# Kernel tuning notes

Measured on AMD Instinct MI355X. Metric: run time of the kernel, lower is better.

Reference implementation:

```python
import jax, jax.numpy as jnp
import numpy as np

B, N, E, H, F, L, S = 4, 384, 768, 32, 3072, 12, 512
D = E // H


def setup_inputs() -> dict:
    key = jax.random.key(0)
    ks = jax.random.split(key, 32)
    inp = {}
    # forward args
    inp['node_type'] = jax.random.randint(ks[0], (B, N, 1), 1, S + 1)  # table has S+1 rows; 0 = pad (unused)
    inp['node_input_feature'] = jax.random.normal(ks[1], (B, N, E), jnp.float32)
    inp['in_degree'] = jax.random.randint(ks[2], (B, N), 0, S)
    inp['out_degree'] = jax.random.randint(ks[3], (B, N), 0, S)
    inp['attn_bias'] = jax.random.normal(ks[4], (B, N, N), jnp.float32) * 0.1
    inp['spatial_pos'] = jax.random.randint(ks[5], (B, N, N), 0, S)
    # embedding tables (normal stddev 0.02, as in the flax module)
    inp['node_emb'] = jax.random.normal(ks[6], (S + 1, E), jnp.float32) * 0.02
    inp['in_deg_emb'] = jax.random.normal(ks[7], (S, E), jnp.float32) * 0.02
    inp['out_deg_emb'] = jax.random.normal(ks[8], (S, E), jnp.float32) * 0.02
    inp['sp_emb'] = jax.random.normal(ks[9], (S, H), jnp.float32) * 0.02
    inp['sp_emb_rev'] = jax.random.normal(ks[10], (S, H), jnp.float32) * 0.02
    # per-layer weights, stacked along leading L axis
    se, sf = 1.0 / np.sqrt(E), 1.0 / np.sqrt(F)
    inp['Wq'] = jax.random.normal(ks[11], (L, E, E), jnp.float32) * se
    inp['bq'] = jax.random.normal(ks[12], (L, E), jnp.float32) * se
    inp['Wk'] = jax.random.normal(ks[13], (L, E, E), jnp.float32) * se
    inp['bk'] = jax.random.normal(ks[14], (L, E), jnp.float32) * se
    inp['Wv'] = jax.random.normal(ks[15], (L, E, E), jnp.float32) * se
    inp['bv'] = jax.random.normal(ks[16], (L, E), jnp.float32) * se
    inp['Wo'] = jax.random.normal(ks[17], (L, E, E), jnp.float32) * se
    inp['bo'] = jnp.zeros((L, E), jnp.float32)
    inp['W1'] = jax.random.normal(ks[18], (L, E, F), jnp.float32) * se
    inp['b1'] = jax.random.normal(ks[19], (L, F), jnp.float32) * se
    inp['W2'] = jax.random.normal(ks[20], (L, F, E), jnp.float32) * sf
    inp['b2'] = jax.random.normal(ks[21], (L, E), jnp.float32) * sf
    inp['ln1_s'] = jnp.ones((L, E), jnp.float32)
    inp['ln1_b'] = jnp.zeros((L, E), jnp.float32)
    inp['ln2_s'] = jnp.ones((L, E), jnp.float32)
    inp['ln2_b'] = jnp.zeros((L, E), jnp.float32)
    return inp


def _layernorm(x, scale, bias, eps=1e-5):
    m = x.mean(-1, keepdims=True)
    v = ((x - m) ** 2).mean(-1, keepdims=True)
    return (x - m) / jnp.sqrt(v + eps) * scale + bias


def _encoder(node_type, node_input_feature, in_degree, out_degree, attn_bias, spatial_pos,
             node_emb, in_deg_emb, out_deg_emb, sp_emb, sp_emb_rev,
             Wq, bq, Wk, bk, Wv, bv, Wo, bo, W1, b1, W2, b2, ln1_s, ln1_b, ln2_s, ln2_b):
    nt = node_type[..., 0]                               # [B,N]
    padding_mask = nt == 0                               # [B,N]
    # node features: node_emb(node_type).sum(-2) + degree embeddings + input feature
    x = (node_emb[node_type].sum(axis=-2)
         + in_deg_emb[in_degree] + out_deg_emb[out_degree]
         + node_input_feature)                           # [B,N,E]
    # spatial attention bias: [B,N,N,H] -> [B,H,N,N], plus graph-level attn_bias
    sb = sp_emb[spatial_pos] + sp_emb_rev[jnp.transpose(spatial_pos, (0, 2, 1))]
    bias = jnp.transpose(sb, (0, 3, 1, 2)) + attn_bias[:, None]  # [B,H,N,N]

    x = jnp.transpose(x, (1, 0, 2))                      # [N,B,E]
    scaling = D ** (-0.5)
    neg_inf = jnp.float32(-jnp.inf)

    def layer(x, p):
        wq, bq_, wk, bk_, wv, bv_, wo, bo_, w1, b1_, w2, b2_, s1, t1, s2, t2 = p
        q = ((x @ wq) + bq_) * scaling                   # [N,B,E], bias scaled too (faithful)
        k = (x @ wk) + bk_
        v = (x @ wv) + bv_
        q = q.reshape(N, B, H, D)
        k = k.reshape(N, B, H, D)
        v = v.reshape(N, B, H, D)
        w = jnp.einsum('nbhd,mbhd->bhnm', q, k) + bias   # [B,H,N,N]
        w = jnp.where(padding_mask[:, None, None, :], neg_inf, w)
        probs = jax.nn.softmax(w.astype(jnp.float32), axis=-1).astype(x.dtype)
        a = jnp.einsum('bhnm,mbhd->nbhd', probs, v).reshape(N, B, E)
        a = a @ wo + bo_
        x = _layernorm(x + a, s1, t1)                    # post-LN
        h = jax.nn.gelu(x @ w1 + b1_)                    # approximate gelu (flax default)
        h = h @ w2 + b2_
        x = _layernorm(x + h, s2, t2)
        return x, None

    xs = (Wq, bq, Wk, bk, Wv, bv, Wo, bo, W1, b1, W2, b2, ln1_s, ln1_b, ln2_s, ln2_b)
    x, _ = jax.lax.scan(layer, x, xs)
    return x                                             # [N,B,E]


def reference(node_type, node_input_feature, in_degree, out_degree, attn_bias, spatial_pos,
              node_emb, in_deg_emb, out_deg_emb, sp_emb, sp_emb_rev,
              Wq, bq, Wk, bk, Wv, bv, Wo, bo, W1, b1, W2, b2, ln1_s, ln1_b, ln2_s, ln2_b):
    return _encoder(node_type, node_input_feature, in_degree, out_degree, attn_bias, spatial_pos,
                    node_emb, in_deg_emb, out_deg_emb, sp_emb, sp_emb_rev,
                    Wq, bq, Wk, bk, Wv, bv, Wo, bo, W1, b1, W2, b2, ln1_s, ln1_b, ln2_s, ln2_b)
```

## Files before the change

### kernel.cpp

```cpp
#include <hip/hip_runtime.h>
#include <hip/hip_bf16.h>

#define Bb 4
#define Nn 384
#define Ee 768
#define Hh 32
#define Ff 3072
#define Ll 12
#define Ss 512
#define Mm (Nn*Bb)

typedef __attribute__((ext_vector_type(8))) short bf16x8;
typedef __attribute__((ext_vector_type(4))) float f32x4;
typedef unsigned short u16;

__device__ __forceinline__ u16 f2b(float f) {
  union { float f; unsigned int i; } c; c.f = f;
  unsigned int x = c.i;
  return (u16)((x + 0x7fffu + ((x >> 16) & 1u)) >> 16);
}
__device__ __forceinline__ float b2f(u16 u) {
  union { unsigned int i; float f; } c; c.i = ((unsigned int)u) << 16; return c.f;
}
__device__ __forceinline__ unsigned pkcvt(float lo, float hi) {
  unsigned r;
  asm("v_cvt_pk_bf16_f32 %0, %1, %2" : "=v"(r) : "v"(lo), "v"(hi));
  return r;
}
__device__ __forceinline__ void gload_lds16(const void* g, void* l) {
  __builtin_amdgcn_global_load_lds((__attribute__((address_space(1))) void*)(g),
                                   (__attribute__((address_space(3))) void*)(l), 16, 0, 0);
}

__global__ __launch_bounds__(256) void embed_kernel(
    const int* __restrict__ node_type, const float* __restrict__ nif,
    const int* __restrict__ in_deg, const int* __restrict__ out_deg,
    const float* __restrict__ node_emb, const float* __restrict__ ind_emb,
    const float* __restrict__ outd_emb,
    float* __restrict__ x, u16* __restrict__ xb)
{
  const int r = blockIdx.x;
  const int n = r / Bb, b = r % Bb;
  const int nt  = node_type[b*Nn + n];
  const int idg = in_deg[b*Nn + n];
  const int odg = out_deg[b*Nn + n];
  for (int c = threadIdx.x; c < Ee; c += 256) {
    float val = node_emb[(size_t)nt*Ee + c] + ind_emb[(size_t)idg*Ee + c]
              + outd_emb[(size_t)odg*Ee + c] + nif[((size_t)b*Nn + n)*Ee + c];
    x[(size_t)r*Ee + c] = val;
    xb[(size_t)r*Ee + c] = f2b(val);
  }
}

__global__ void spT_kernel(const int* __restrict__ sp, int* __restrict__ spT)
{
  __shared__ int tile[32][33];
  const int b = blockIdx.z;
  const int n0 = blockIdx.y * 32, m0 = blockIdx.x * 32;
  const int tx = threadIdx.x, ty = threadIdx.y;
  for (int i = ty; i < 32; i += 8)
    tile[i][tx] = sp[((size_t)b*Nn + n0 + i)*Nn + m0 + tx];
  __syncthreads();
  for (int i = ty; i < 32; i += 8)
    spT[((size_t)b*Nn + m0 + i)*Nn + n0 + tx] = tile[tx][i];
}

__global__ __launch_bounds__(256) void bias_pre_kernel(
    const float* __restrict__ atb, const int* __restrict__ sp, const int* __restrict__ spT,
    const float* __restrict__ sp_emb, const float* __restrict__ sp_emb_rev,
    u16* __restrict__ biasb)
{
  __shared__ float spc[512], sprc[512];
  const int bx = blockIdx.x, h = blockIdx.y, b = blockIdx.z;
  const int t = threadIdx.x;
  for (int i = t; i < 512; i += 256) {
    spc[i]  = sp_emb[(size_t)i*Hh + h];
    sprc[i] = sp_emb_rev[(size_t)i*Hh + h];
  }
  __syncthreads();
  const int q = bx*16 + ((t >> 2) & 15);
  const size_t rowb = ((size_t)b*Nn + q)*Nn;
  u16* outb = biasb + (((size_t)(b*Hh + h)*24 + bx)*24)*256 + t;
  const int mbase = ((t >> 6) << 2) + (t & 3);
  for (int tt = 0; tt < 24; ++tt) {
    const int m = tt*16 + mbase;
    float v = atb[rowb + m] + spc[sp[rowb + m]] + sprc[spT[rowb + m]];
    outb[tt*256] = f2b(v);
  }
}

__global__ __launch_bounds__(256) void wconv_kernel(
    const float* __restrict__ Wq, const float* __restrict__ Wk, const float* __restrict__ Wv,
    const float* __restrict__ Wo, const float* __restrict__ W1, const float* __restrict__ W2,
    int layer0, u16* __restrict__ wTall, unsigned slotStride)
{
  __shared__ float tile[64][68];
  const int layer = layer0 + blockIdx.y;
  u16* slot = wTall + (size_t)blockIdx.y * slotStride;
  int tid = blockIdx.x;
  const float* src; u16* dst; int Ns, Ks;
  if (tid < 432)       { int seg = tid / 144; tid -= seg*144;
                         src = (seg==0?Wq:(seg==1?Wk:Wv)) + (size_t)layer*Ee*Ee;
                         dst = slot + (size_t)seg*589824; Ns = 768; Ks = 768; }
  else if (tid < 576)  { tid -= 432; src = Wo + (size_t)layer*Ee*Ee; dst = slot + 1769472; Ns = 768;  Ks = 768; }
  else if (tid < 1152) { tid -= 576; src = W1 + (size_t)layer*Ee*Ff; dst = slot + 2359296; Ns = 3072; Ks = 768; }
  else                 { tid -= 1152; src = W2 + (size_t)layer*Ff*Ee; dst = slot + 4718592; Ns = 768; Ks = 3072; }
  const int tc = Ns >> 6;
  const int tk = tid / tc, tn = tid % tc;
  const int t = threadIdx.x;
  #pragma unroll
  for (int i = 0; i < 4; ++i) {
    const int id = t + i*256;
    const int r = id >> 4, c = (id & 15) << 2;
    *(float4*)&tile[r][c] = *(const float4*)(src + (size_t)(tk*64 + r)*Ns + tn*64 + c);
  }
  __syncthreads();
  #pragma unroll
  for (int i = 0; i < 2; ++i) {
    const int ch = t + i*256;
    const int n = ch >> 3, kc = (ch & 7) << 3;
    uint4 u;
    u.x = pkcvt(tile[kc+0][n], tile[kc+1][n]);
    u.y = pkcvt(tile[kc+2][n], tile[kc+3][n]);
    u.z = pkcvt(tile[kc+4][n], tile[kc+5][n]);
    u.w = pkcvt(tile[kc+6][n], tile[kc+7][n]);
    *(uint4*)(dst + (size_t)(tn*64 + n)*Ks + tk*64 + kc) = u;
  }
}

template<int EPI>
__global__ __launch_bounds__(256) void gemm3_kernel(
    const u16* __restrict__ A, const u16* __restrict__ Bw,
    const float* __restrict__ b0, const float* __restrict__ b1, const float* __restrict__ b2,
    int Kfull, int Kc, float scaleQ,
    float* __restrict__ outF, u16* __restrict__ outB)
{
  __shared__ __align__(16) u16 As[2][64][64];
  __shared__ __align__(16) u16 Bs[2][64][64];
  const int t = threadIdx.x, lane = t & 63, wave = t >> 6;
  int bx = blockIdx.x, by = blockIdx.y;
  {
    const int gx = gridDim.x;
    const int nwg = gx * gridDim.y;
    const int bid = bx + gx * by;
    const int cpx = nwg >> 3;
    const int s = (bid & 7) * cpx + (bid >> 3);
    bx = s % gx; by = s / gx;
  }
  const int m0 = bx * 64, n0 = by * 64;
  const int k0 = blockIdx.z * Kc;
  const int wm = wave >> 1, wn = wave & 1;
  const int ql = lane & 15, hi = lane >> 4;
  const int nk = Kc >> 6;
  const int sr = t >> 3;
  const int sslot = (t & 7) ^ (sr & 7);
  const size_t aoff = (size_t)(m0 + sr)*Kfull + k0 + (sslot << 3);
  const size_t boff = (size_t)(n0 + sr)*Kfull + k0 + (sslot << 3);
  const size_t rstep = (size_t)32 * Kfull;

  f32x4 acc[2][2];
  #pragma unroll
  for (int a = 0; a < 2; ++a)
    #pragma unroll
    for (int c = 0; c < 2; ++c) acc[a][c] = (f32x4){0.f,0.f,0.f,0.f};

  gload_lds16(A + aoff,         (char*)&As[0][0][0] + t*16);
  gload_lds16(A + aoff + rstep, (char*)&As[0][0][0] + 4096 + t*16);
  gload_lds16(Bw + boff,         (char*)&Bs[0][0][0] + t*16);
  gload_lds16(Bw + boff + rstep, (char*)&Bs[0][0][0] + 4096 + t*16);

  for (int kt = 0; kt < nk; ++kt) {
    const int cur = kt & 1, nxt = cur ^ 1;
    const bool pre = (kt + 1 < nk);
    if (pre) {
      const size_t kk = (size_t)(kt + 1) << 6;
      gload_lds16(A + aoff + kk,         (char*)&As[nxt][0][0] + t*16);
      gload_lds16(A + aoff + kk + rstep, (char*)&As[nxt][0][0] + 4096 + t*16);
      gload_lds16(Bw + boff + kk,         (char*)&Bs[nxt][0][0] + t*16);
      gload_lds16(Bw + boff + kk + rstep, (char*)&Bs[nxt][0][0] + 4096 + t*16);
      asm volatile("s_waitcnt vmcnt(4)" ::: "memory");
    } else {
      asm volatile("s_waitcnt vmcnt(0)" ::: "memory");
    }
    __builtin_amdgcn_s_barrier();
    __builtin_amdgcn_sched_barrier(0);

    const char* aBase = (const char*)&As[cur][0][0];
    const char* bBase = (const char*)&Bs[cur][0][0];
    bf16x8 af[2][2], bf[2][2];
    #pragma unroll
    for (int f = 0; f < 2; ++f)
      #pragma unroll
      for (int ks = 0; ks < 2; ++ks) {
        const int row = wm*32 + f*16 + ql;
        af[f][ks] = *(const bf16x8*)(aBase + row*128 + ((((ks<<2)+hi) ^ (ql&7)) << 4));
      }
    #pragma unroll
    for (int f = 0; f < 2; ++f)
      #pragma unroll
      for (int ks = 0; ks < 2; ++ks) {
        const int row = wn*32 + f*16 + ql;
        bf[f][ks] = *(const bf16x8*)(bBase + row*128 + ((((ks<<2)+hi) ^ (ql&7)) << 4));
      }
    #pragma unroll
    for (int ks = 0; ks < 2; ++ks)
      #pragma unroll
      for (int fm = 0; fm < 2; ++fm)
        #pragma unroll
        for (int fn = 0; fn < 2; ++fn)
          acc[fm][fn] = __builtin_amdgcn_mfma_f32_16x16x32_bf16(af[fm][ks], bf[fn][ks], acc[fm][fn], 0, 0, 0);
    if (pre) {
      __builtin_amdgcn_sched_barrier(0);
      __builtin_amdgcn_s_barrier();
    }
  }

  #pragma unroll
  for (int fm = 0; fm < 2; ++fm) {
    const int rowb = m0 + wm*32 + fm*16 + hi*4;
    #pragma unroll
    for (int fn = 0; fn < 2; ++fn) {
      const int gcol = n0 + wn*32 + fn*16 + ql;
      float bv, scale = 1.0f;
      if (EPI == 0) {
        const int seg = gcol / 768;
        const int cw = gcol - seg*768;
        bv = (seg == 0) ? b0[cw] : ((seg == 1) ? b1[cw] : b2[cw]);
        if (seg == 0) scale = scaleQ;
      } else if (EPI == 1) {
        bv = (blockIdx.z == 0) ? b0[gcol] : 0.0f;
      } else {
        bv = b0[gcol];
      }
      f32x4 v = acc[fm][fn];
      #pragma unroll
      for (int j = 0; j < 4; ++j) {
        float val = (v[j] + bv) * scale;
        if (EPI == 0) {
          outB[(size_t)(rowb + j) * 2304 + gcol] = f2b(val);
        } else if (EPI == 1) {
          outF[(size_t)blockIdx.z * (Mm*768) + (size_t)(rowb + j) * 768 + gcol] = val;
        } else {
          float arg = 0.7978845608028654f * (val + 0.044715f * val * val * val);
          float e = __expf(2.0f * arg);
          float g = 0.5f * val * (2.0f - 2.0f / (e + 1.0f));
          outB[(size_t)(rowb + j) * 3072 + gcol] = f2b(g);
        }
      }
    }
  }
}

template<int PREBIAS>
__global__ __launch_bounds__(256) void attn2_kernel(
    const u16* __restrict__ qkv,
    const u16* __restrict__ biasb,
    const float* __restrict__ atb, const int* __restrict__ sp, const int* __restrict__ spT,
    const float* __restrict__ sp_emb, const float* __restrict__ sp_emb_rev,
    u16* __restrict__ ab)
{
  __shared__ __align__(16) u16 Kt[384][32];
  __shared__ __align__(16) u16 Vt[32][392];
  __shared__ __align__(16) u16 Qt[64][32];
  __shared__ __align__(16) u16 Pw[4][16][32];
  __shared__ float spc[512], sprc[512];
  const int bid = blockIdx.x;
  const int ntile = bid % 6;
  const int h = (bid / 6) % Hh;
  const int b = bid / (6 * Hh);
  const int t = threadIdx.x, lane = t & 63, wave = t >> 6;
  const int ql = lane & 15, hi = lane >> 4;

  for (int idx = t; idx < 384*6; idx += 256) {
    const int m = idx / 6, c = idx - m*6;
    const u16* base = qkv + ((size_t)m*Bb + b)*2304 + h*24 + c*4;
    uint2 kk = *(const uint2*)(base + 768);
    uint2 vv = *(const uint2*)(base + 1536);
    *(uint2*)&Kt[m][c*4] = kk;
    Vt[c*4+0][m] = (u16)(vv.x & 0xffffu); Vt[c*4+1][m] = (u16)(vv.x >> 16);
    Vt[c*4+2][m] = (u16)(vv.y & 0xffffu); Vt[c*4+3][m] = (u16)(vv.y >> 16);
  }
  for (int idx = t; idx < 384*2; idx += 256)
    *(uint2*)&Kt[idx>>1][24 + (idx&1)*4] = make_uint2(0u, 0u);
  for (int idx = t; idx < 8*196; idx += 256)
    *(unsigned*)((char*)&Vt[24][0] + idx*4) = 0u;
  for (int idx = t; idx < 64*6; idx += 256) {
    const int qr = idx / 6, c = idx - qr*6;
    const u16* base = qkv + ((size_t)(ntile*64 + qr)*Bb + b)*2304 + h*24 + c*4;
    *(uint2*)&Qt[qr][c*4] = *(const uint2*)base;
  }
  for (int idx = t; idx < 64*2; idx += 256)
    *(uint2*)&Qt[idx>>1][24 + (idx&1)*4] = make_uint2(0u, 0u);
  if (!PREBIAS) {
    for (int i = t; i < 512; i += 256) {
      spc[i]  = sp_emb[(size_t)i*Hh + h];
      sprc[i] = sp_emb_rev[(size_t)i*Hh + h];
    }
  }
  __syncthreads();

  const int q0 = ntile*64 + wave*16;
  const int q = q0 + ql;
  const bf16x8 qf = *(const bf16x8*)&Qt[wave*16 + ql][hi*8];

  f32x4 f[24];
  const u16* bp = biasb + (((size_t)(b*Hh + h)*24 + ntile*4 + wave)*24)*256 + lane*4;
  const size_t crow = ((size_t)b*Nn + q)*Nn;
  #pragma unroll
  for (int tt = 0; tt < 24; ++tt) {
    bf16x8 kf = *(const bf16x8*)&Kt[tt*16 + ql][hi*8];
    f32x4 z = (f32x4){0.f,0.f,0.f,0.f};
    f32x4 s = __builtin_amdgcn_mfma_f32_16x16x32_bf16(kf, qf, z, 0, 0, 0);
    if (PREBIAS) {
      uint2 bb = *(const uint2*)(bp + tt*256);
      s[0] += b2f((u16)(bb.x & 0xffffu)); s[1] += b2f((u16)(bb.x >> 16));
      s[2] += b2f((u16)(bb.y & 0xffffu)); s[3] += b2f((u16)(bb.y >> 16));
    } else {
      const int off = tt*16 + hi*4;
      int4 s4 = *(const int4*)(sp + crow + off);
      int4 t4 = *(const int4*)(spT + crow + off);
      float4 a4 = *(const float4*)(atb + crow + off);
      s[0] += a4.x + spc[s4.x] + sprc[t4.x];
      s[1] += a4.y + spc[s4.y] + sprc[t4.y];
      s[2] += a4.z + spc[s4.z] + sprc[t4.z];
      s[3] += a4.w + spc[s4.w] + sprc[t4.w];
    }
    f[tt] = s;
  }

  float mx = -3.0e38f;
  #pragma unroll
  for (int tt = 0; tt < 24; ++tt)
    mx = fmaxf(mx, fmaxf(fmaxf(f[tt][0], f[tt][1]), fmaxf(f[tt][2], f[tt][3])));
  mx = fmaxf(mx, __shfl_xor(mx, 16, 64));
  mx = fmaxf(mx, __shfl_xor(mx, 32, 64));
  float sum = 0.f;
  #pragma unroll
  for (int tt = 0; tt < 24; ++tt) {
    #pragma unroll
    for (int j = 0; j < 4; ++j) { f[tt][j] = __expf(f[tt][j] - mx); sum += f[tt][j]; }
  }
  sum += __shfl_xor(sum, 16, 64);
  sum += __shfl_xor(sum, 32, 64);
  const float inv = 1.0f / sum;

  f32x4 o0 = (f32x4){0.f,0.f,0.f,0.f}, o1 = (f32x4){0.f,0.f,0.f,0.f};
  char* prow = (char*)&Pw[wave][ql][0];
  const int swz = (ql & 3) << 4;
  #pragma unroll
  for (int c = 0; c < 12; ++c) {
    unsigned w0 = pkcvt(f[2*c][0],   f[2*c][1]);
    unsigned w1 = pkcvt(f[2*c][2],   f[2*c][3]);
    unsigned w2 = pkcvt(f[2*c+1][0], f[2*c+1][1]);
    unsigned w3 = pkcvt(f[2*c+1][2], f[2*c+1][3]);
    *(unsigned*)(prow + (((hi*8)      ) ^ swz)) = w0;
    *(unsigned*)(prow + (((hi*8) +  4) ^ swz)) = w1;
    *(unsigned*)(prow + (((hi*8) + 32) ^ swz)) = w2;
    *(unsigned*)(prow + (((hi*8) + 36) ^ swz)) = w3;
    bf16x8 a = *(const bf16x8*)(prow + ((hi*16) ^ swz));
    bf16x8 v0 = *(const bf16x8*)&Vt[ql][c*32 + hi*8];
    bf16x8 v1 = *(const bf16x8*)&Vt[16 + ql][c*32 + hi*8];
    o0 = __builtin_amdgcn_mfma_f32_16x16x32_bf16(a, v0, o0, 0, 0, 0);
    o1 = __builtin_amdgcn_mfma_f32_16x16x32_bf16(a, v1, o1, 0, 0, 0);
  }

  #pragma unroll
  for (int j = 0; j < 4; ++j) {
    float invj = __shfl(inv, hi*4 + j, 64);
    const int qg = q0 + hi*4 + j;
    u16* orow = ab + ((size_t)qg*Bb + b)*Ee + h*24;
    orow[ql] = f2b(o0[j] * invj);
    if (ql < 8) orow[16 + ql] = f2b(o1[j] * invj);
  }
}

template<int NP>
__global__ __launch_bounds__(256) void ln_kernel(
    const float* __restrict__ xin, const float* __restrict__ delta,
    const float* __restrict__ gamma, const float* __restrict__ beta,
    float* __restrict__ xout, u16* __restrict__ xb)
{
  __shared__ float red[8];
  const int r = blockIdx.x, t = threadIdx.x;
  const size_t base = (size_t)r * Ee;
  float v[3];
  #pragma unroll
  for (int i = 0; i < 3; ++i) {
    int c = t + i*256;
    float d = xin[base + c];
    #pragma unroll
    for (int p = 0; p < NP; ++p) d += delta[(size_t)p*(Mm*768) + base + c];
    v[i] = d;
  }
  float s = v[0] + v[1] + v[2];
  #pragma unroll
  for (int off = 1; off < 64; off <<= 1) s += __shfl_xor(s, off, 64);
  if ((t & 63) == 0) red[t >> 6] = s;
  __syncthreads();
  const float mean = (red[0] + red[1] + red[2] + red[3]) * (1.0f / 768.0f);
  float qs = 0.f;
  #pragma unroll
  for (int i = 0; i < 3; ++i) { float d = v[i] - mean; qs += d * d; }
  #pragma unroll
  for (int off = 1; off < 64; off <<= 1) qs += __shfl_xor(qs, off, 64);
  if ((t & 63) == 0) red[4 + (t >> 6)] = qs;
  __syncthreads();
  const float var = (red[4] + red[5] + red[6] + red[7]) * (1.0f / 768.0f);
  const float rstd = rsqrtf(var + 1e-5f);
  #pragma unroll
  for (int i = 0; i < 3; ++i) {
    int c = t + i*256;
    float o = (v[i] - mean) * rstd * gamma[c] + beta[c];
    xout[base + c] = o;
    xb[base + c] = f2b(o);
  }
}

extern "C" void kernel_launch(void* const* d_in, const int* in_sizes, int n_in,
                              void* d_out, int out_size, void* d_ws, size_t ws_size,
                              hipStream_t stream) {
  const int*   node_type  = (const int*)d_in[0];
  const float* nif        = (const float*)d_in[1];
  const int*   in_deg     = (const int*)d_in[2];
  const int*   out_deg    = (const int*)d_in[3];
  const float* atb        = (const float*)d_in[4];
  const int*   sp         = (const int*)d_in[5];
  const float* node_emb   = (const float*)d_in[6];
  const float* ind_emb    = (const float*)d_in[7];
  const float* outd_emb   = (const float*)d_in[8];
  const float* sp_emb     = (const float*)d_in[9];
  const float* sp_emb_rev = (const float*)d_in[10];
  const float* Wq = (const float*)d_in[11]; const float* bq = (const float*)d_in[12];
  const float* Wk = (const float*)d_in[13]; const float* bk = (const float*)d_in[14];
  const float* Wv = (const float*)d_in[15]; const float* bv = (const float*)d_in[16];
  const float* Wo = (const float*)d_in[17]; const float* bo = (const float*)d_in[18];
  const float* W1 = (const float*)d_in[19]; const float* b1 = (const float*)d_in[20];
  const float* W2 = (const float*)d_in[21]; const float* b2 = (const float*)d_in[22];
  const float* ln1s = (const float*)d_in[23]; const float* ln1b = (const float*)d_in[24];
  const float* ln2s = (const float*)d_in[25]; const float* ln2b = (const float*)d_in[26];

  char* ws = (char*)d_ws;
  float* x      = (float*)(ws);
  u16*   xb     = (u16*)(ws +  4718592);
  u16*   qkvb16 = (u16*)(ws +  7077888);
  u16*   abuf   = (u16*)(ws + 14155776);
  u16*   hb     = (u16*)(ws + 16515072);
  float* obufP  = (float*)(ws + 25952256);
  int*   spTb   = (int*)(ws + 44826624);
  u16*   biasb  = (u16*)(ws + 47185920);
  const bool useBias = ws_size >= 99090432ull;
  const bool allW    = ws_size >= 254803968ull;
  u16* wTall = (u16*)(ws + (useBias ? 84934656 : 47185920));
  const unsigned LSLOT = 7077888u;

  embed_kernel<<<Mm, 256, 0, stream>>>(node_type, nif, in_deg, out_deg,
                                       node_emb, ind_emb, outd_emb, x, xb);
  spT_kernel<<<dim3(12, 12, 4), dim3(32, 8), 0, stream>>>(sp, spTb);
  if (useBias)
    bias_pre_kernel<<<dim3(24, 32, 4), 256, 0, stream>>>(atb, sp, spTb, sp_emb, sp_emb_rev, biasb);
  if (allW)
    wconv_kernel<<<dim3(1728, 12), 256, 0, stream>>>(Wq, Wk, Wv, Wo, W1, W2,
                                                     0, wTall, LSLOT);

  const float scaleQ = 0.2041241452319315f;

  for (int l = 0; l < Ll; ++l) {
    const float *bql = bq + (size_t)l*Ee, *bkl = bk + (size_t)l*Ee, *bvl = bv + (size_t)l*Ee;
    const float *bol = bo + (size_t)l*Ee;
    const float *b1l = b1 + (size_t)l*Ff, *b2l = b2 + (size_t)l*Ee;

    if (!allW)
      wconv_kernel<<<dim3(1728, 1), 256, 0, stream>>>(Wq, Wk, Wv, Wo, W1, W2,
                                                      l, wTall, 0u);
    u16* slot = wTall + (size_t)(allW ? l : 0) * LSLOT;
    const u16* qkvT = slot;
    const u16* woT  = slot + 1769472;
    const u16* w1T  = slot + 2359296;
    const u16* w2T  = slot + 4718592;

    gemm3_kernel<0><<<dim3(24, 36), 256, 0, stream>>>(xb, qkvT, bql, bkl, bvl,
                                                      768, 768, scaleQ, nullptr, qkvb16);
    if (useBias)
      attn2_kernel<1><<<768, 256, 0, stream>>>(qkvb16, biasb, atb, sp, spTb,
                                               sp_emb, sp_emb_rev, abuf);
    else
      attn2_kernel<0><<<768, 256, 0, stream>>>(qkvb16, nullptr, atb, sp, spTb,
                                               sp_emb, sp_emb_rev, abuf);
    gemm3_kernel<1><<<dim3(24, 12, 2), 256, 0, stream>>>(abuf, woT, bol, bol, bol,
                                                         768, 384, 1.0f, obufP, nullptr);
    ln_kernel<2><<<Mm, 256, 0, stream>>>(x, obufP, ln1s + (size_t)l*Ee, ln1b + (size_t)l*Ee, x, xb);
    gemm3_kernel<2><<<dim3(24, 48), 256, 0, stream>>>(xb, w1T, b1l, b1l, b1l,
                                                      768, 768, 1.0f, nullptr, hb);
    gemm3_kernel<1><<<dim3(24, 12, 4), 256, 0, stream>>>(hb, w2T, b2l, b2l, b2l,
                                                         3072, 768, 1.0f, obufP, nullptr);
    float* xdst = (l == Ll - 1) ? (float*)d_out : x;
    ln_kernel<4><<<Mm, 256, 0, stream>>>(x, obufP, ln2s + (size_t)l*Ee, ln2b + (size_t)l*Ee, xdst, xb);
  }
}
```

Baseline: 1.409 ms.

## Enlarge GEMM M-tile to 128 and process two query tiles per attention block

The GEMM kernel doubles its M tile from 64 to 128 rows, giving each wave a 64x32 sub-tile with precomputed LDS offsets, and halves the grid x-dimension of all four GEMM launches. The attention kernel now handles two 64-query tiles per block, reusing the K/V tiles already staged in LDS, so half as many blocks are launched. The weight-conversion tile padding also changes from 68 to 65 with scalar stores. The intent is more reuse of B operands and K/V loads per block, at the cost of more registers and fewer blocks, which may under-fill the GPU on smaller grids.

```diff
diff --git a/kernel.cpp b/kernel.cpp
--- a/kernel.cpp
+++ b/kernel.cpp
@@ -94,7 +94,7 @@
     const float* __restrict__ Wo, const float* __restrict__ W1, const float* __restrict__ W2,
     int layer0, u16* __restrict__ wTall, unsigned slotStride)
 {
-  __shared__ float tile[64][68];
+  __shared__ float tile[64][65];
   const int layer = layer0 + blockIdx.y;
   u16* slot = wTall + (size_t)blockIdx.y * slotStride;
   int tid = blockIdx.x;
@@ -112,7 +112,8 @@
   for (int i = 0; i < 4; ++i) {
     const int id = t + i*256;
     const int r = id >> 4, c = (id & 15) << 2;
-    *(float4*)&tile[r][c] = *(const float4*)(src + (size_t)(tk*64 + r)*Ns + tn*64 + c);
+    float4 v = *(const float4*)(src + (size_t)(tk*64 + r)*Ns + tn*64 + c);
+    tile[r][c+0] = v.x; tile[r][c+1] = v.y; tile[r][c+2] = v.z; tile[r][c+3] = v.w;
   }
   __syncthreads();
   #pragma unroll
@@ -135,7 +136,7 @@
     int Kfull, int Kc, float scaleQ,
     float* __restrict__ outF, u16* __restrict__ outB)
 {
-  __shared__ __align__(16) u16 As[2][64][64];
+  __shared__ __align__(16) u16 As[2][128][64];
   __shared__ __align__(16) u16 Bs[2][64][64];
   const int t = threadIdx.x, lane = t & 63, wave = t >> 6;
   int bx = blockIdx.x, by = blockIdx.y;
@@ -147,7 +148,7 @@
     const int s = (bid & 7) * cpx + (bid >> 3);
     bx = s % gx; by = s / gx;
   }
-  const int m0 = bx * 64, n0 = by * 64;
+  const int m0 = bx * 128, n0 = by * 64;
   const int k0 = blockIdx.z * Kc;
   const int wm = wave >> 1, wn = wave & 1;
   const int ql = lane & 15, hi = lane >> 4;
@@ -158,27 +159,41 @@
   const size_t boff = (size_t)(n0 + sr)*Kfull + k0 + (sslot << 3);
   const size_t rstep = (size_t)32 * Kfull;
 
-  f32x4 acc[2][2];
-  #pragma unroll
-  for (int a = 0; a < 2; ++a)
+  int aro[4][2], bro[2][2];
+  #pragma unroll
+  for (int ks = 0; ks < 2; ++ks) {
+    const int kb = (((ks<<2) + hi) ^ (ql & 7)) << 4;
+    #pragma unroll
+    for (int f = 0; f < 4; ++f) aro[f][ks] = (wm*64 + f*16 + ql)*128 + kb;
+    #pragma unroll
+    for (int f = 0; f < 2; ++f) bro[f][ks] = (wn*32 + f*16 + ql)*128 + kb;
+  }
+
+  f32x4 acc[4][2];
+  #pragma unroll
+  for (int a = 0; a < 4; ++a)
     #pragma unroll
     for (int c = 0; c < 2; ++c) acc[a][c] = (f32x4){0.f,0.f,0.f,0.f};
 
-  gload_lds16(A + aoff,         (char*)&As[0][0][0] + t*16);
-  gload_lds16(A + aoff + rstep, (char*)&As[0][0][0] + 4096 + t*16);
-  gload_lds16(Bw + boff,         (char*)&Bs[0][0][0] + t*16);
-  gload_lds16(Bw + boff + rstep, (char*)&Bs[0][0][0] + 4096 + t*16);
+  #pragma unroll
+  for (int i = 0; i < 4; ++i)
+    gload_lds16(A + aoff + i*rstep, (char*)&As[0][0][0] + i*4096 + t*16);
+  #pragma unroll
+  for (int i = 0; i < 2; ++i)
+    gload_lds16(Bw + boff + i*rstep, (char*)&Bs[0][0][0] + i*4096 + t*16);
 
   for (int kt = 0; kt < nk; ++kt) {
     const int cur = kt & 1, nxt = cur ^ 1;
     const bool pre = (kt + 1 < nk);
     if (pre) {
       const size_t kk = (size_t)(kt + 1) << 6;
-      gload_lds16(A + aoff + kk,         (char*)&As[nxt][0][0] + t*16);
-      gload_lds16(A + aoff + kk + rstep, (char*)&As[nxt][0][0] + 4096 + t*16);
-      gload_lds16(Bw + boff + kk,         (char*)&Bs[nxt][0][0] + t*16);
-      gload_lds16(Bw + boff + kk + rstep, (char*)&Bs[nxt][0][0] + 4096 + t*16);
-      asm volatile("s_waitcnt vmcnt(4)" ::: "memory");
+      #pragma unroll
+      for (int i = 0; i < 4; ++i)
+        gload_lds16(A + aoff + kk + i*rstep, (char*)&As[nxt][0][0] + i*4096 + t*16);
+      #pragma unroll
+      for (int i = 0; i < 2; ++i)
+        gload_lds16(Bw + boff + kk + i*rstep, (char*)&Bs[nxt][0][0] + i*4096 + t*16);
+      asm volatile("s_waitcnt vmcnt(6)" ::: "memory");
     } else {
       asm volatile("s_waitcnt vmcnt(0)" ::: "memory");
     }
@@ -187,25 +202,21 @@
 
     const char* aBase = (const char*)&As[cur][0][0];
     const char* bBase = (const char*)&Bs[cur][0][0];
-    bf16x8 af[2][2], bf[2][2];
+    bf16x8 af[4][2], bf[2][2];
+    #pragma unroll
+    for (int f = 0; f < 4; ++f)
+      #pragma unroll
+      for (int ks = 0; ks < 2; ++ks)
+        af[f][ks] = *(const bf16x8*)(aBase + aro[f][ks]);
     #pragma unroll
     for (int f = 0; f < 2; ++f)
       #pragma unroll
-      for (int ks = 0; ks < 2; ++ks) {
-        const int row = wm*32 + f*16 + ql;
-        af[f][ks] = *(const bf16x8*)(aBase + row*128 + ((((ks<<2)+hi) ^ (ql&7)) << 4));
-      }
-    #pragma unroll
-    for (int f = 0; f < 2; ++f)
-      #pragma unroll
-      for (int ks = 0; ks < 2; ++ks) {
-        const int row = wn*32 + f*16 + ql;
-        bf[f][ks] = *(const bf16x8*)(bBase + row*128 + ((((ks<<2)+hi) ^ (ql&7)) << 4));
-      }
+      for (int ks = 0; ks < 2; ++ks)
+        bf[f][ks] = *(const bf16x8*)(bBase + bro[f][ks]);
     #pragma unroll
     for (int ks = 0; ks < 2; ++ks)
       #pragma unroll
-      for (int fm = 0; fm < 2; ++fm)
+      for (int fm = 0; fm < 4; ++fm)
         #pragma unroll
         for (int fn = 0; fn < 2; ++fn)
           acc[fm][fn] = __builtin_amdgcn_mfma_f32_16x16x32_bf16(af[fm][ks], bf[fn][ks], acc[fm][fn], 0, 0, 0);
@@ -216,8 +227,8 @@
   }
 
   #pragma unroll
-  for (int fm = 0; fm < 2; ++fm) {
-    const int rowb = m0 + wm*32 + fm*16 + hi*4;
+  for (int fm = 0; fm < 4; ++fm) {
+    const int rowb = m0 + wm*64 + fm*16 + hi*4;
     #pragma unroll
     for (int fn = 0; fn < 2; ++fn) {
       const int gcol = n0 + wn*32 + fn*16 + ql;
@@ -265,9 +276,9 @@
   __shared__ __align__(16) u16 Pw[4][16][32];
   __shared__ float spc[512], sprc[512];
   const int bid = blockIdx.x;
-  const int ntile = bid % 6;
-  const int h = (bid / 6) % Hh;
-  const int b = bid / (6 * Hh);
+  const int pair = bid % 3;
+  const int h = (bid / 3) % Hh;
+  const int b = bid / (3 * Hh);
   const int t = threadIdx.x, lane = t & 63, wave = t >> 6;
   const int ql = lane & 15, hi = lane >> 4;
 
@@ -284,93 +295,98 @@
     *(uint2*)&Kt[idx>>1][24 + (idx&1)*4] = make_uint2(0u, 0u);
   for (int idx = t; idx < 8*196; idx += 256)
     *(unsigned*)((char*)&Vt[24][0] + idx*4) = 0u;
-  for (int idx = t; idx < 64*6; idx += 256) {
-    const int qr = idx / 6, c = idx - qr*6;
-    const u16* base = qkv + ((size_t)(ntile*64 + qr)*Bb + b)*2304 + h*24 + c*4;
-    *(uint2*)&Qt[qr][c*4] = *(const uint2*)base;
-  }
-  for (int idx = t; idx < 64*2; idx += 256)
-    *(uint2*)&Qt[idx>>1][24 + (idx&1)*4] = make_uint2(0u, 0u);
   if (!PREBIAS) {
     for (int i = t; i < 512; i += 256) {
       spc[i]  = sp_emb[(size_t)i*Hh + h];
       sprc[i] = sp_emb_rev[(size_t)i*Hh + h];
     }
   }
-  __syncthreads();
-
-  const int q0 = ntile*64 + wave*16;
-  const int q = q0 + ql;
-  const bf16x8 qf = *(const bf16x8*)&Qt[wave*16 + ql][hi*8];
-
-  f32x4 f[24];
-  const u16* bp = biasb + (((size_t)(b*Hh + h)*24 + ntile*4 + wave)*24)*256 + lane*4;
-  const size_t crow = ((size_t)b*Nn + q)*Nn;
-  #pragma unroll
-  for (int tt = 0; tt < 24; ++tt) {
-    bf16x8 kf = *(const bf16x8*)&Kt[tt*16 + ql][hi*8];
-    f32x4 z = (f32x4){0.f,0.f,0.f,0.f};
-    f32x4 s = __builtin_amdgcn_mfma_f32_16x16x32_bf16(kf, qf, z, 0, 0, 0);
-    if (PREBIAS) {
-      uint2 bb = *(const uint2*)(bp + tt*256);
-      s[0] += b2f((u16)(bb.x & 0xffffu)); s[1] += b2f((u16)(bb.x >> 16));
-      s[2] += b2f((u16)(bb.y & 0xffffu)); s[3] += b2f((u16)(bb.y >> 16));
-    } else {
-      const int off = tt*16 + hi*4;
-      int4 s4 = *(const int4*)(sp + crow + off);
-      int4 t4 = *(const int4*)(spT + crow + off);
-      float4 a4 = *(const float4*)(atb + crow + off);
-      s[0] += a4.x + spc[s4.x] + sprc[t4.x];
-      s[1] += a4.y + spc[s4.y] + sprc[t4.y];
-      s[2] += a4.z + spc[s4.z] + sprc[t4.z];
-      s[3] += a4.w + spc[s4.w] + sprc[t4.w];
-    }
-    f[tt] = s;
-  }
-
-  float mx = -3.0e38f;
-  #pragma unroll
-  for (int tt = 0; tt < 24; ++tt)
-    mx = fmaxf(mx, fmaxf(fmaxf(f[tt][0], f[tt][1]), fmaxf(f[tt][2], f[tt][3])));
-  mx = fmaxf(mx, __shfl_xor(mx, 16, 64));
-  mx = fmaxf(mx, __shfl_xor(mx, 32, 64));
-  float sum = 0.f;
-  #pragma unroll
-  for (int tt = 0; tt < 24; ++tt) {
-    #pragma unroll
-    for (int j = 0; j < 4; ++j) { f[tt][j] = __expf(f[tt][j] - mx); sum += f[tt][j]; }
-  }
-  sum += __shfl_xor(sum, 16, 64);
-  sum += __shfl_xor(sum, 32, 64);
-  const float inv = 1.0f / sum;
-
-  f32x4 o0 = (f32x4){0.f,0.f,0.f,0.f}, o1 = (f32x4){0.f,0.f,0.f,0.f};
-  char* prow = (char*)&Pw[wave][ql][0];
-  const int swz = (ql & 3) << 4;
-  #pragma unroll
-  for (int c = 0; c < 12; ++c) {
-    unsigned w0 = pkcvt(f[2*c][0],   f[2*c][1]);
-    unsigned w1 = pkcvt(f[2*c][2],   f[2*c][3]);
-    unsigned w2 = pkcvt(f[2*c+1][0], f[2*c+1][1]);
-    unsigned w3 = pkcvt(f[2*c+1][2], f[2*c+1][3]);
-    *(unsigned*)(prow + (((hi*8)      ) ^ swz)) = w0;
-    *(unsigned*)(prow + (((hi*8) +  4) ^ swz)) = w1;
-    *(unsigned*)(prow + (((hi*8) + 32) ^ swz)) = w2;
-    *(unsigned*)(prow + (((hi*8) + 36) ^ swz)) = w3;
-    bf16x8 a = *(const bf16x8*)(prow + ((hi*16) ^ swz));
-    bf16x8 v0 = *(const bf16x8*)&Vt[ql][c*32 + hi*8];
-    bf16x8 v1 = *(const bf16x8*)&Vt[16 + ql][c*32 + hi*8];
-    o0 = __builtin_amdgcn_mfma_f32_16x16x32_bf16(a, v0, o0, 0, 0, 0);
-    o1 = __builtin_amdgcn_mfma_f32_16x16x32_bf16(a, v1, o1, 0, 0, 0);
-  }
-
-  #pragma unroll
-  for (int j = 0; j < 4; ++j) {
-    float invj = __shfl(inv, hi*4 + j, 64);
-    const int qg = q0 + hi*4 + j;
-    u16* orow = ab + ((size_t)qg*Bb + b)*Ee + h*24;
-    orow[ql] = f2b(o0[j] * invj);
-    if (ql < 8) orow[16 + ql] = f2b(o1[j] * invj);
+
+  for (int qi = 0; qi < 2; ++qi) {
+    const int ntile = pair*2 + qi;
+    for (int idx = t; idx < 64*6; idx += 256) {
+      const int qr = idx / 6, c = idx - qr*6;
+      const u16* base = qkv + ((size_t)(ntile*64 + qr)*Bb + b)*2304 + h*24 + c*4;
+      *(uint2*)&Qt[qr][c*4] = *(const uint2*)base;
+    }
+    for (int idx = t; idx < 64*2; idx += 256)
+      *(uint2*)&Qt[idx>>1][24 + (idx&1)*4] = make_uint2(0u, 0u);
+    __syncthreads();
+
+    const int q0 = ntile*64 + wave*16;
+    const int q = q0 + ql;
+    const bf16x8 qf = *(const bf16x8*)&Qt[wave*16 + ql][hi*8];
+
+    f32x4 f[24];
+    const u16* bp = biasb + (((size_t)(b*Hh + h)*24 + ntile*4 + wave)*24)*256 + lane*4;
+    const size_t crow = ((size_t)b*Nn + q)*Nn;
+    #pragma unroll
+    for (int tt = 0; tt < 24; ++tt) {
+      bf16x8 kf = *(const bf16x8*)&Kt[tt*16 + ql][hi*8];
+      f32x4 z = (f32x4){0.f,0.f,0.f,0.f};
+      f32x4 s = __builtin_amdgcn_mfma_f32_16x16x32_bf16(kf, qf, z, 0, 0, 0);
+      if (PREBIAS) {
+        uint2 bb = *(const uint2*)(bp + tt*256);
+        s[0] += b2f((u16)(bb.x & 0xffffu)); s[1] += b2f((u16)(bb.x >> 16));
+        s[2] += b2f((u16)(bb.y & 0xffffu)); s[3] += b2f((u16)(bb.y >> 16));
+      } else {
+        const int off = tt*16 + hi*4;
+        int4 s4 = *(const int4*)(sp + crow + off);
+        int4 t4 = *(const int4*)(spT + crow + off);
+        float4 a4 = *(const float4*)(atb + crow + off);
+        s[0] += a4.x + spc[s4.x] + sprc[t4.x];
+        s[1] += a4.y + spc[s4.y] + sprc[t4.y];
+        s[2] += a4.z + spc[s4.z] + sprc[t4.z];
+        s[3] += a4.w + spc[s4.w] + sprc[t4.w];
+      }
+      f[tt] = s;
+    }
+
+    float mx = -3.0e38f;
+    #pragma unroll
+    for (int tt = 0; tt < 24; ++tt)
+      mx = fmaxf(mx, fmaxf(fmaxf(f[tt][0], f[tt][1]), fmaxf(f[tt][2], f[tt][3])));
+    mx = fmaxf(mx, __shfl_xor(mx, 16, 64));
+    mx = fmaxf(mx, __shfl_xor(mx, 32, 64));
+    float sum = 0.f;
+    #pragma unroll
+    for (int tt = 0; tt < 24; ++tt) {
+      #pragma unroll
+      for (int j = 0; j < 4; ++j) { f[tt][j] = __expf(f[tt][j] - mx); sum += f[tt][j]; }
+    }
+    sum += __shfl_xor(sum, 16, 64);
+    sum += __shfl_xor(sum, 32, 64);
+    const float inv = 1.0f / sum;
+
+    f32x4 o0 = (f32x4){0.f,0.f,0.f,0.f}, o1 = (f32x4){0.f,0.f,0.f,0.f};
+    char* prow = (char*)&Pw[wave][ql][0];
+    const int swz = (ql & 3) << 4;
+    #pragma unroll
+    for (int c = 0; c < 12; ++c) {
+      unsigned w0 = pkcvt(f[2*c][0],   f[2*c][1]);
+      unsigned w1 = pkcvt(f[2*c][2],   f[2*c][3]);
+      unsigned w2 = pkcvt(f[2*c+1][0], f[2*c+1][1]);
+      unsigned w3 = pkcvt(f[2*c+1][2], f[2*c+1][3]);
+      *(unsigned*)(prow + (((hi*8)      ) ^ swz)) = w0;
+      *(unsigned*)(prow + (((hi*8) +  4) ^ swz)) = w1;
+      *(unsigned*)(prow + (((hi*8) + 32) ^ swz)) = w2;
+      *(unsigned*)(prow + (((hi*8) + 36) ^ swz)) = w3;
+      bf16x8 a = *(const bf16x8*)(prow + ((hi*16) ^ swz));
+      bf16x8 v0 = *(const bf16x8*)&Vt[ql][c*32 + hi*8];
+      bf16x8 v1 = *(const bf16x8*)&Vt[16 + ql][c*32 + hi*8];
+      o0 = __builtin_amdgcn_mfma_f32_16x16x32_bf16(a, v0, o0, 0, 0, 0);
+      o1 = __builtin_amdgcn_mfma_f32_16x16x32_bf16(a, v1, o1, 0, 0, 0);
+    }
+
+    #pragma unroll
+    for (int j = 0; j < 4; ++j) {
+      float invj = __shfl(inv, hi*4 + j, 64);
+      const int qg = q0 + hi*4 + j;
+      u16* orow = ab + ((size_t)qg*Bb + b)*Ee + h*24;
+      orow[ql] = f2b(o0[j] * invj);
+      if (ql < 8) orow[16 + ql] = f2b(o1[j] * invj);
+    }
+    __syncthreads();
   }
 }
 
@@ -478,20 +494,20 @@
     const u16* w1T  = slot + 2359296;
     const u16* w2T  = slot + 4718592;
 
-    gemm3_kernel<0><<<dim3(24, 36), 256, 0, stream>>>(xb, qkvT, bql, bkl, bvl,
+    gemm3_kernel<0><<<dim3(12, 36), 256, 0, stream>>>(xb, qkvT, bql, bkl, bvl,
                                                       768, 768, scaleQ, nullptr, qkvb16);
     if (useBias)
-      attn2_kernel<1><<<768, 256, 0, stream>>>(qkvb16, biasb, atb, sp, spTb,
+      attn2_kernel<1><<<384, 256, 0, stream>>>(qkvb16, biasb, atb, sp, spTb,
                                                sp_emb, sp_emb_rev, abuf);
     else
-      attn2_kernel<0><<<768, 256, 0, stream>>>(qkvb16, nullptr, atb, sp, spTb,
+      attn2_kernel<0><<<384, 256, 0, stream>>>(qkvb16, nullptr, atb, sp, spTb,
                                                sp_emb, sp_emb_rev, abuf);
-    gemm3_kernel<1><<<dim3(24, 12, 2), 256, 0, stream>>>(abuf, woT, bol, bol, bol,
+    gemm3_kernel<1><<<dim3(12, 12, 2), 256, 0, stream>>>(abuf, woT, bol, bol, bol,
                                                          768, 384, 1.0f, obufP, nullptr);
     ln_kernel<2><<<Mm, 256, 0, stream>>>(x, obufP, ln1s + (size_t)l*Ee, ln1b + (size_t)l*Ee, x, xb);
-    gemm3_kernel<2><<<dim3(24, 48), 256, 0, stream>>>(xb, w1T, b1l, b1l, b1l,
+    gemm3_kernel<2><<<dim3(12, 48), 256, 0, stream>>>(xb, w1T, b1l, b1l, b1l,
                                                       768, 768, 1.0f, nullptr, hb);
-    gemm3_kernel<1><<<dim3(24, 12, 4), 256, 0, stream>>>(hb, w2T, b2l, b2l, b2l,
+    gemm3_kernel<1><<<dim3(12, 12, 4), 256, 0, stream>>>(hb, w2T, b2l, b2l, b2l,
                                                          3072, 768, 1.0f, obufP, nullptr);
     float* xdst = (l == Ll - 1) ? (float*)d_out : x;
     ln_kernel<4><<<Mm, 256, 0, stream>>>(x, obufP, ln2s + (size_t)l*Ee, ln2b + (size_t)l*Ee, xdst, xb);
```

Measured after the change: 1.347 ms. -4.4%, faster.
